# Optimization experiments

Measured on AMD Instinct MI355X. Metric: run time of the kernel, lower is better.

The kernel has to match this reference:

```python
import jax, jax.numpy as jnp
import numpy as np

N_NODES = 50000
N_EDGES = 400000
NUM_FEAT = 11
HID = 64
LAT = 64
HEADS = 3
MAX_NODES = 29
NUM_GRAPHS = 2048
NEG_SLOPE = 0.2


def _w(key, shape):
    return (jax.random.normal(key, shape) * 0.05).astype(jnp.float32)


def setup_inputs() -> dict:
    key = jax.random.key(0)
    ks = jax.random.split(key, 32)
    x = jax.random.normal(ks[0], (N_NODES, NUM_FEAT), dtype=jnp.float32)
    edge_index = jax.random.randint(ks[1], (2, N_EDGES), 0, N_NODES, dtype=jnp.int64)
    batch = jnp.sort(jax.random.randint(ks[2], (N_NODES,), 0, NUM_GRAPHS, dtype=jnp.int64))
    d = {"x": x, "edge_index": edge_index, "batch": batch}
    # GATv2 layer params: lin_l, lin_r ([in, heads*out]), att [heads,out], bias [out]
    dims = [(NUM_FEAT, HID), (HID, 2 * HID), (2 * HID, 4 * HID)]
    k = 3
    for i, (cin, cout) in enumerate(dims, start=1):
        d[f"Wl{i}"] = _w(ks[k], (cin, HEADS * cout)); k += 1
        d[f"bl{i}"] = jnp.zeros((HEADS * cout,), jnp.float32)
        d[f"Wr{i}"] = _w(ks[k], (cin, HEADS * cout)); k += 1
        d[f"br{i}"] = jnp.zeros((HEADS * cout,), jnp.float32)
        d[f"att{i}"] = _w(ks[k], (HEADS, cout)); k += 1
        d[f"b{i}"] = jnp.zeros((cout,), jnp.float32)
    d["Wmu"] = _w(ks[k], (4 * HID, LAT)); k += 1
    d["bmu"] = jnp.zeros((LAT,), jnp.float32)
    d["Wlv"] = _w(ks[k], (4 * HID, LAT)); k += 1
    d["blv"] = jnp.zeros((LAT,), jnp.float32)
    out_dim = MAX_NODES * NUM_FEAT + MAX_NODES * MAX_NODES
    d["Wd1"] = _w(ks[k], (LAT, 4 * HID)); k += 1
    d["bd1"] = jnp.zeros((4 * HID,), jnp.float32)
    d["Wd2"] = _w(ks[k], (4 * HID, 8 * HID)); k += 1
    d["bd2"] = jnp.zeros((8 * HID,), jnp.float32)
    d["Wd3"] = _w(ks[k], (8 * HID, out_dim)); k += 1
    d["bd3"] = jnp.zeros((out_dim,), jnp.float32)
    return d


def _gatv2(x, src, dst, Wl, bl, Wr, br, att, bias):
    # GATv2Conv, heads=HEADS, concat=False (mean over heads), self-loops already in src/dst
    N = x.shape[0]
    H, C = att.shape
    xl = (x @ Wl + bl).reshape(N, H, C)  # source transform
    xr = (x @ Wr + br).reshape(N, H, C)  # target transform
    e = jax.nn.leaky_relu(xl[src] + xr[dst], NEG_SLOPE)  # [E,H,C]
    logits = jnp.einsum('ehc,hc->eh', e, att)            # [E,H]
    mx = jax.ops.segment_max(logits, dst, num_segments=N)
    a = jnp.exp(logits - mx[dst])
    denom = jax.ops.segment_sum(a, dst, num_segments=N)
    alpha = a / (denom[dst] + 1e-16)
    out = jax.ops.segment_sum(alpha[:, :, None] * xl[src], dst, num_segments=N)  # [N,H,C]
    return out.mean(axis=1) + bias


def reference(x, edge_index, batch,
              Wl1, bl1, Wr1, br1, att1, b1,
              Wl2, bl2, Wr2, br2, att2, b2,
              Wl3, bl3, Wr3, br3, att3, b3,
              Wmu, bmu, Wlv, blv,
              Wd1, bd1, Wd2, bd2, Wd3, bd3):
    N = x.shape[0]
    loops = jnp.arange(N, dtype=edge_index.dtype)
    src = jnp.concatenate([edge_index[0], loops])
    dst = jnp.concatenate([edge_index[1], loops])
    h = jax.nn.relu(_gatv2(x, src, dst, Wl1, bl1, Wr1, br1, att1, b1))
    h = jax.nn.relu(_gatv2(h, src, dst, Wl2, bl2, Wr2, br2, att2, b2))
    h = jax.nn.relu(_gatv2(h, src, dst, Wl3, bl3, Wr3, br3, att3, b3))
    g = jax.ops.segment_sum(h, batch, num_segments=NUM_GRAPHS)  # global_add_pool
    mu = g @ Wmu + bmu
    logvar = g @ Wlv + blv
    z = mu  # deterministic decode of the posterior mean (no forward() given)
    o = jax.nn.relu(z @ Wd1 + bd1)
    o = jax.nn.relu(o @ Wd2 + bd2)
    o = o @ Wd3 + bd3
    nsplit = MAX_NODES * NUM_FEAT
    x_rec = o[:, :nsplit].reshape(-1, MAX_NODES, NUM_FEAT)
    adj = o[:, nsplit:].reshape(-1, MAX_NODES, MAX_NODES)
    adj_rec = (adj + jnp.swapaxes(adj, 1, 2)) / 2
    return (x_rec, adj_rec, mu, logvar)
```

## Files before the change

### kernel.cpp

```cpp
#include <hip/hip_runtime.h>
#include <hip/hip_bf16.h>

typedef __hip_bfloat16 bf16;
typedef unsigned short ushortT;
typedef ushortT u16x2 __attribute__((ext_vector_type(2)));
typedef ushortT u16x4 __attribute__((ext_vector_type(4)));
typedef ushortT u16x8 __attribute__((ext_vector_type(8)));
typedef __bf16   bf16x8 __attribute__((ext_vector_type(8)));
typedef float    f32x4  __attribute__((ext_vector_type(4)));

#define N_NODES    50000
#define E_EDGES    400000
#define E_TOT      450000
#define NUM_GRAPHS 2048
#define SCAN_CHUNK 1024
#define N_CHUNKS   ((N_NODES + SCAN_CHUNK - 1) / SCAN_CHUNK)

__device__ __forceinline__ float fromb(ushortT u) {
    unsigned int i = ((unsigned int)u) << 16;
    return __builtin_bit_cast(float, i);
}
__device__ __forceinline__ ushortT tob(float v) {
    bf16 h = __float2bfloat16(v);
    return __builtin_bit_cast(ushortT, h);
}

template <int VEC> struct RawV;
template <> struct RawV<1> { using T = ushortT; };
template <> struct RawV<2> { using T = u16x2; };
template <> struct RawV<4> { using T = u16x4; };

__device__ __forceinline__ void cvtv(ushortT r, float* f) { f[0] = fromb(r); }
__device__ __forceinline__ void cvtv(u16x2 r, float* f)   { f[0] = fromb(r.x); f[1] = fromb(r.y); }
__device__ __forceinline__ void cvtv(u16x4 r, float* f)   { f[0] = fromb(r.x); f[1] = fromb(r.y);
                                                            f[2] = fromb(r.z); f[3] = fromb(r.w); }

__global__ void diag_kernel(float* out, float v) { if (threadIdx.x == 0) out[0] = v; }

__global__ void hist_kernel(const int* __restrict__ ei, int* __restrict__ counts) {
    int e = blockIdx.x * 256 + threadIdx.x;
    if (e >= E_TOT) return;
    int d = (e < E_EDGES) ? ei[E_EDGES + e] : (e - E_EDGES);
    atomicAdd(&counts[d], 1);
}

__global__ __launch_bounds__(256) void scan_sums(const int* __restrict__ counts,
                                                 int* __restrict__ chunk_sums) {
    __shared__ int red[4];
    int base = blockIdx.x * SCAN_CHUNK;
    int t = threadIdx.x;
    int s = 0;
    #pragma unroll
    for (int i = 0; i < 4; i++) {
        int idx = base + t + i * 256;
        if (idx < N_NODES) s += counts[idx];
    }
    #pragma unroll
    for (int o = 32; o > 0; o >>= 1) s += __shfl_xor(s, o);
    if ((t & 63) == 0) red[t >> 6] = s;
    __syncthreads();
    if (t == 0) chunk_sums[blockIdx.x] = red[0] + red[1] + red[2] + red[3];
}

__global__ __launch_bounds__(64) void scan_chunks(const int* __restrict__ chunk_sums,
                                                  int* __restrict__ chunk_base) {
    int t = threadIdx.x;
    int v = (t < N_CHUNKS) ? chunk_sums[t] : 0;
    int orig = v;
    #pragma unroll
    for (int o = 1; o < 64; o <<= 1) {
        int u = __shfl_up(v, o);
        if (t >= o) v += u;
    }
    if (t < N_CHUNKS) chunk_base[t] = v - orig;
}

__global__ __launch_bounds__(256) void scan_write(const int* __restrict__ counts,
                                                  const int* __restrict__ chunk_base,
                                                  int* __restrict__ offsets) {
    __shared__ int wsum[4];
    int chunk = blockIdx.x;
    int base = chunk * SCAN_CHUNK;
    int t = threadIdx.x;
    int lane = t & 63, w = t >> 6;

    int c[4];
    int e0 = base + t * 4;
    #pragma unroll
    for (int k = 0; k < 4; k++) {
        int idx = e0 + k;
        c[k] = (idx < N_NODES) ? counts[idx] : 0;
    }
    int local = c[0] + c[1] + c[2] + c[3];

    int v = local;
    #pragma unroll
    for (int o = 1; o < 64; o <<= 1) {
        int u = __shfl_up(v, o);
        if (lane >= o) v += u;
    }
    if (lane == 63) wsum[w] = v;
    __syncthreads();
    int wbase = 0;
    for (int i = 0; i < w; i++) wbase += wsum[i];

    int run = chunk_base[chunk] + wbase + (v - local);
    #pragma unroll
    for (int k = 0; k < 4; k++) {
        int idx = e0 + k;
        if (idx < N_NODES) offsets[idx] = run;
        run += c[k];
    }
    if (chunk == 0 && t == 0) offsets[N_NODES] = E_TOT;
}

__global__ void copy_kernel(const int* __restrict__ src, int* __restrict__ dst, int n) {
    int i = blockIdx.x * 256 + threadIdx.x;
    if (i < n) dst[i] = src[i];
}

__global__ void scatter_kernel(const int* __restrict__ ei, int* __restrict__ cursor,
                               int* __restrict__ srcs) {
    int e = blockIdx.x * 256 + threadIdx.x;
    if (e >= E_TOT) return;
    int s, d;
    if (e < E_EDGES) { s = ei[e]; d = ei[E_EDGES + e]; }
    else             { s = d = e - E_EDGES; }
    int pos = atomicAdd(&cursor[d], 1);
    srcs[pos] = s;
}

__global__ void repack_kernel(const float* __restrict__ W, ushortT* __restrict__ Bp,
                              int K, int N) {
    int idx = blockIdx.x * 256 + threadIdx.x;
    if (idx >= K * N) return;
    int k = idx / N, n = idx % N;
    Bp[((size_t)(k >> 3) * N + n) * 8 + (k & 7)] = tob(W[idx]);
}

__global__ void repack_split(const float* __restrict__ W, ushortT* __restrict__ Bh,
                             ushortT* __restrict__ Bl, int K, int N, int Npad) {
    int idx = blockIdx.x * 256 + threadIdx.x;
    if (idx >= K * Npad) return;
    int k = idx / Npad, n = idx % Npad;
    float v = (n < N) ? W[(size_t)k * N + n] : 0.f;
    ushortT h = tob(v);
    float r = v - fromb(h);
    size_t o = ((size_t)(k >> 3) * Npad + n) * 8 + (k & 7);
    Bh[o] = h;
    Bl[o] = tob(r);
}

__global__ __launch_bounds__(192) void l1_transform(const float* __restrict__ x,
                                                    const float* __restrict__ Wl,
                                                    const float* __restrict__ bl,
                                                    const float* __restrict__ Wr,
                                                    const float* __restrict__ br,
                                                    ushortT* __restrict__ XL,
                                                    ushortT* __restrict__ XR, int M) {
    __shared__ float xs[64][11];
    const int tid = threadIdx.x;
    const int bm  = blockIdx.x * 64;
    const int rows = (M - bm < 64) ? (M - bm) : 64;

    float wl[11], wr[11];
    #pragma unroll
    for (int k = 0; k < 11; k++) {
        wl[k] = Wl[k * 192 + tid];
        wr[k] = Wr[k * 192 + tid];
    }
    float blc = bl[tid], brc = br[tid];

    for (int i = tid; i < rows * 11; i += 192)
        xs[i / 11][i % 11] = x[(size_t)bm * 11 + i];
    __syncthreads();

    for (int r = 0; r < rows; r++) {
        float al = blc, ar = brc;
        #pragma unroll
        for (int k = 0; k < 11; k++) {
            float xv = xs[r][k];
            al += xv * wl[k];
            ar += xv * wr[k];
        }
        size_t o = (size_t)(bm + r) * 192 + tid;
        XL[o] = tob(al);
        XR[o] = tob(ar);
    }
}

template <bool RELU>
__global__ __launch_bounds__(256) void gemm_dec(const float* __restrict__ A,
                                                const float* __restrict__ B,
                                                const float* __restrict__ bias,
                                                float* __restrict__ C,
                                                int M, int N, int K,
                                                int lda, int ldb, int ldc) {
    __shared__ float As[32][33];
    __shared__ float Bs[32][65];
    int tid = threadIdx.x;
    int tm = tid >> 4, tn = tid & 15;
    int bm = blockIdx.y * 32, bn = blockIdx.x * 64;
    float acc[2][4] = {};
    for (int k0 = 0; k0 < K; k0 += 32) {
        #pragma unroll
        for (int i = 0; i < 4; i++) {
            int e = tid + i * 256;
            int r = e >> 5, k = e & 31;
            int row = bm + r, kk = k0 + k;
            float v = 0.f;
            if (row < M && kk < K) v = A[(size_t)row * lda + kk];
            As[k][r] = v;
        }
        #pragma unroll
        for (int i = 0; i < 8; i++) {
            int e = tid + i * 256;
            int k = e >> 6, n = e & 63;
            int kk = k0 + k, col = bn + n;
            float v = 0.f;
            if (kk < K && col < N) v = B[(size_t)kk * ldb + col];
            Bs[k][n] = v;
        }
        __syncthreads();
        #pragma unroll
        for (int k = 0; k < 32; k++) {
            float a0 = As[k][tm * 2 + 0], a1 = As[k][tm * 2 + 1];
            float b0 = Bs[k][tn * 4 + 0], b1 = Bs[k][tn * 4 + 1];
            float b2 = Bs[k][tn * 4 + 2], b3 = Bs[k][tn * 4 + 3];
            acc[0][0] += a0 * b0; acc[0][1] += a0 * b1; acc[0][2] += a0 * b2; acc[0][3] += a0 * b3;
            acc[1][0] += a1 * b0; acc[1][1] += a1 * b1; acc[1][2] += a1 * b2; acc[1][3] += a1 * b3;
        }
        __syncthreads();
    }
    #pragma unroll
    for (int i = 0; i < 2; i++) {
        int row = bm + tm * 2 + i;
        if (row >= M) continue;
        #pragma unroll
        for (int j = 0; j < 4; j++) {
            int col = bn + tn * 4 + j;
            if (col >= N) continue;
            float v = acc[i][j] + bias[col];
            if (RELU) v = fmaxf(v, 0.f);
            C[(size_t)row * ldc + col] = v;
        }
    }
}

template <bool RELU>
__global__ __launch_bounds__(256) void mfma_dec(const float* __restrict__ A,
                                                const ushortT* __restrict__ Bh,
                                                const ushortT* __restrict__ Bl,
                                                const float* __restrict__ bias,
                                                float* __restrict__ C,
                                                int M, int N, int K, int Npad,
                                                int lda, int ldc) {
    __shared__ ushortT Ah[4 * 128 * 8];
    __shared__ ushortT Al[4 * 128 * 8];
    const int tid = threadIdx.x;
    const int bm = blockIdx.y * 128;
    const int bn = blockIdx.x * 128;
    const int lane = tid & 63;
    const int l15 = lane & 15, lg = lane >> 4;
    const int wid = tid >> 6;
    const int wm = wid >> 1, wn = wid & 1;

    f32x4 acc[4][4] = {};

    for (int k0 = 0; k0 < K; k0 += 32) {
        __syncthreads();
        #pragma unroll
        for (int it = 0; it < 2; it++) {
            int c = tid + it * 256;
            int row = c >> 2, kg = c & 3;
            const float* ap = A + (size_t)(bm + row) * lda + k0 + kg * 8;
            u16x8 hv, lv;
            #pragma unroll
            for (int i = 0; i < 8; i++) {
                float v = ap[i];
                ushortT h = tob(v);
                hv[i] = h;
                lv[i] = tob(v - fromb(h));
            }
            int unit = (kg * 128 + row) ^ kg;
            *reinterpret_cast<u16x8*>(&Ah[unit * 8]) = hv;
            *reinterpret_cast<u16x8*>(&Al[unit * 8]) = lv;
        }
        __syncthreads();

        bf16x8 ah[4], al[4], bhf[4], blf[4];
        #pragma unroll
        for (int mf = 0; mf < 4; mf++) {
            int row = wm * 64 + mf * 16 + l15;
            int unit = (lg * 128 + row) ^ lg;
            ah[mf] = __builtin_bit_cast(bf16x8, *reinterpret_cast<const u16x8*>(&Ah[unit * 8]));
            al[mf] = __builtin_bit_cast(bf16x8, *reinterpret_cast<const u16x8*>(&Al[unit * 8]));
        }
        int kgG = (k0 >> 3) + lg;
        #pragma unroll
        for (int nf = 0; nf < 4; nf++) {
            int n = bn + wn * 64 + nf * 16 + l15;
            size_t o = ((size_t)kgG * Npad + n) * 8;
            bhf[nf] = __builtin_bit_cast(bf16x8, *reinterpret_cast<const u16x8*>(Bh + o));
            blf[nf] = __builtin_bit_cast(bf16x8, *reinterpret_cast<const u16x8*>(Bl + o));
        }
        #pragma unroll
        for (int mf = 0; mf < 4; mf++) {
            #pragma unroll
            for (int nf = 0; nf < 4; nf++) {
                acc[mf][nf] = __builtin_amdgcn_mfma_f32_16x16x32_bf16(ah[mf], bhf[nf], acc[mf][nf], 0, 0, 0);
                acc[mf][nf] = __builtin_amdgcn_mfma_f32_16x16x32_bf16(ah[mf], blf[nf], acc[mf][nf], 0, 0, 0);
                acc[mf][nf] = __builtin_amdgcn_mfma_f32_16x16x32_bf16(al[mf], bhf[nf], acc[mf][nf], 0, 0, 0);
            }
        }
    }

    #pragma unroll
    for (int nf = 0; nf < 4; nf++) {
        int col = bn + wn * 64 + nf * 16 + l15;
        if (col >= N) continue;
        float bv = bias[col];
        #pragma unroll
        for (int mf = 0; mf < 4; mf++) {
            #pragma unroll
            for (int q = 0; q < 4; q++) {
                int row = bm + wm * 64 + mf * 16 + lg * 4 + q;
                if (row < M) {
                    float v = acc[mf][nf][q] + bv;
                    if (RELU) v = fmaxf(v, 0.f);
                    C[(size_t)row * ldc + col] = v;
                }
            }
        }
    }
}

template <int K, int CHH>
__global__ __launch_bounds__(256) void mfma_gemm(const ushortT* __restrict__ A,
                                                 const ushortT* __restrict__ BpL,
                                                 const ushortT* __restrict__ BpR,
                                                 const float* __restrict__ bl,
                                                 const float* __restrict__ br,
                                                 bf16* __restrict__ XL,
                                                 bf16* __restrict__ XR,
                                                 int M, int Nfull, int n0) {
    constexpr int KU = K / 8;
    __shared__ ushortT Alds[KU * 128 * 8];
    const int tid = threadIdx.x;
    const int bm  = blockIdx.y * 128;
    const int bnb = blockIdx.x * 128;

    for (int u = tid; u < 128 * KU; u += 256) {
        int row = u / KU, kg = u % KU;
        int rg = bm + row; if (rg > M - 1) rg = M - 1;
        u16x8 v = *reinterpret_cast<const u16x8*>(A + (size_t)rg * K + kg * 8);
        int unit = (kg * 128 + row) ^ (kg & 7);
        *reinterpret_cast<u16x8*>(&Alds[unit * 8]) = v;
    }
    __syncthreads();

    const int lane = tid & 63;
    const int l15 = lane & 15, lg = lane >> 4;
    const int wid = tid >> 6;
    const int wm = wid >> 1, wn = wid & 1;

    f32x4 acc[4][4] = {};
    #pragma unroll
    for (int s = 0; s < K / 32; s++) {
        int kg = s * 4 + lg;
        bf16x8 a[4], b[4];
        #pragma unroll
        for (int mf = 0; mf < 4; mf++) {
            int row = wm * 64 + mf * 16 + l15;
            int unit = (kg * 128 + row) ^ (kg & 7);
            a[mf] = __builtin_bit_cast(bf16x8,
                    *reinterpret_cast<const u16x8*>(&Alds[unit * 8]));
        }
        #pragma unroll
        for (int nf = 0; nf < 4; nf++) {
            int cb = bnb + wn * 64 + nf * 16;
            const ushortT* bp; int n;
            if (cb < CHH) { bp = BpL; n = n0 + cb + l15; }
            else          { bp = BpR; n = n0 + cb - CHH + l15; }
            b[nf] = __builtin_bit_cast(bf16x8,
                    *reinterpret_cast<const u16x8*>(bp + ((size_t)kg * Nfull + n) * 8));
        }
        #pragma unroll
        for (int mf = 0; mf < 4; mf++)
            #pragma unroll
            for (int nf = 0; nf < 4; nf++)
                acc[mf][nf] = __builtin_amdgcn_mfma_f32_16x16x32_bf16(
                    a[mf], b[nf], acc[mf][nf], 0, 0, 0);
    }

    #pragma unroll
    for (int nf = 0; nf < 4; nf++) {
        int cb = bnb + wn * 64 + nf * 16;
        bf16* Cp; const float* bs; int c;
        if (cb < CHH) { Cp = XL; bs = bl; c = cb + l15; }
        else          { Cp = XR; bs = br; c = cb - CHH + l15; }
        float bv = bs[c];
        #pragma unroll
        for (int mf = 0; mf < 4; mf++) {
            #pragma unroll
            for (int q = 0; q < 4; q++) {
                int r = bm + wm * 64 + mf * 16 + lg * 4 + q;
                if (r < M) Cp[(size_t)r * CHH + c] = __float2bfloat16(acc[mf][nf][q] + bv);
            }
        }
    }
}

template <int CHH, int MODE>
__global__ __launch_bounds__(256) void gat_head(const ushortT* __restrict__ XL,
                                                const ushortT* __restrict__ XR,
                                                int ldx, int offx,
                                                const float* __restrict__ att_h,
                                                const float* __restrict__ bias,
                                                const int* __restrict__ offsets,
                                                const int* __restrict__ srcs,
                                                ushortT* __restrict__ OUT, int N) {
    constexpr int VEC = CHH / 64;
    using RT = typename RawV<VEC>::T;
    int wid  = threadIdx.x >> 6;
    int lane = threadIdx.x & 63;
    int n = blockIdx.x * 4 + wid;
    if (n >= N) return;

    float xr_[VEC], a06[VEC], a04[VEC], acc[VEC];
    const ushortT* xrp = XR + (size_t)n * ldx + offx + VEC * lane;
    #pragma unroll
    for (int i = 0; i < VEC; i++) {
        xr_[i] = fromb(xrp[i]);
        float a = att_h[VEC * lane + i];
        a06[i] = 0.6f * a;
        a04[i] = 0.4f * a;
        acc[i] = 0.f;
    }
    float denom = 0.f;

    const int e0 = offsets[n], e1 = offsets[n + 1];
    const int deg = e1 - e0;
    const int loff = offx + VEC * lane;

    for (int base = 0; base < deg; base += 64) {
        int cnt = deg - base; if (cnt > 64) cnt = 64;
        int sl = srcs[e0 + base + ((lane < cnt) ? lane : (cnt - 1))];

        RT pf0, pf1, pf2, pf3;
        pf0 = *reinterpret_cast<const RT*>(XL + (size_t)__shfl(sl, 0) * ldx + loff);
        pf1 = (cnt > 1) ? *reinterpret_cast<const RT*>(XL + (size_t)__shfl(sl, 1) * ldx + loff) : pf0;
        pf2 = (cnt > 2) ? *reinterpret_cast<const RT*>(XL + (size_t)__shfl(sl, 2) * ldx + loff) : pf0;
        pf3 = (cnt > 3) ? *reinterpret_cast<const RT*>(XL + (size_t)__shfl(sl, 3) * ldx + loff) : pf0;

        for (int j = 0; j < cnt; ++j) {
            RT cur = pf0;
            pf0 = pf1; pf1 = pf2; pf2 = pf3;
            if (j + 4 < cnt)
                pf3 = *reinterpret_cast<const RT*>(XL + (size_t)__shfl(sl, j + 4) * ldx + loff);

            float xl[VEC];
            cvtv(cur, xl);
            float part = 0.f;
            #pragma unroll
            for (int i = 0; i < VEC; i++) {
                float v = xl[i] + xr_[i];
                float av = fabsf(v);
                part = fmaf(a06[i], v, part);
                part = fmaf(a04[i], av, part);
            }
            #pragma unroll
            for (int ofs = 32; ofs > 0; ofs >>= 1)
                part += __shfl_xor(part, ofs);

            float w = __expf(part);
            denom += w;
            #pragma unroll
            for (int i = 0; i < VEC; i++) acc[i] = fmaf(w, xl[i], acc[i]);
        }
    }

    float inv = 1.f / (denom + 1e-16f);
    #pragma unroll
    for (int i = 0; i < VEC; i++) {
        int c = VEC * lane + i;
        size_t idx = (size_t)n * CHH + c;
        float v = acc[i] * inv;
        if (MODE > 0) v += fromb(OUT[idx]);
        if (MODE == 2) { v = v * (1.f / 3.f) + bias[c]; v = fmaxf(v, 0.f); }
        OUT[idx] = tob(v);
    }
}

__global__ void pool_kernel(const ushortT* __restrict__ h3, const int* __restrict__ batch,
                            float* __restrict__ G) {
    int g = blockIdx.x;
    int c = threadIdx.x;
    int lo = 0, hi = N_NODES;
    while (lo < hi) { int mid = (lo + hi) >> 1; if (batch[mid] < g) lo = mid + 1; else hi = mid; }
    int s0 = lo;
    hi = N_NODES;
    while (lo < hi) { int mid = (lo + hi) >> 1; if (batch[mid] < g + 1) lo = mid + 1; else hi = mid; }
    int s1 = lo;
    float sum = 0.f;
    for (int n = s0; n < s1; n++) sum += fromb(h3[(size_t)n * 256 + c]);
    G[(size_t)g * 256 + c] = sum;
}

__global__ void assemble_kernel(const float* __restrict__ o3, float* __restrict__ out) {
    int g = blockIdx.x;
    const float* row = o3 + (size_t)g * 1160;
    float* xrec = out + (size_t)g * 319;
    for (int p = threadIdx.x; p < 319; p += 256) xrec[p] = row[p];
    float* adj = out + 653312 + (size_t)g * 841;
    for (int p = threadIdx.x; p < 841; p += 256) {
        int i = p / 29, j = p % 29;
        adj[p] = 0.5f * (row[319 + p] + row[319 + j * 29 + i]);
    }
}

extern "C" void kernel_launch(void* const* d_in, const int* in_sizes, int n_in,
                              void* d_out, int out_size, void* d_ws, size_t ws_size,
                              hipStream_t stream) {
    const float* x     = (const float*)d_in[0];
    const int*   ei    = (const int*)d_in[1];
    const int*   batch = (const int*)d_in[2];
    const float* Wl1 = (const float*)d_in[3];
    const float* bl1 = (const float*)d_in[4];
    const float* Wr1 = (const float*)d_in[5];
    const float* br1 = (const float*)d_in[6];
    const float* att1= (const float*)d_in[7];
    const float* b1  = (const float*)d_in[8];
    const float* Wl2 = (const float*)d_in[9];
    const float* bl2 = (const float*)d_in[10];
    const float* Wr2 = (const float*)d_in[11];
    const float* br2 = (const float*)d_in[12];
    const float* att2= (const float*)d_in[13];
    const float* b2  = (const float*)d_in[14];
    const float* Wl3 = (const float*)d_in[15];
    const float* bl3 = (const float*)d_in[16];
    const float* Wr3 = (const float*)d_in[17];
    const float* br3 = (const float*)d_in[18];
    const float* att3= (const float*)d_in[19];
    const float* b3  = (const float*)d_in[20];
    const float* Wmu = (const float*)d_in[21];
    const float* bmu = (const float*)d_in[22];
    const float* Wlv = (const float*)d_in[23];
    const float* blv = (const float*)d_in[24];
    const float* Wd1 = (const float*)d_in[25];
    const float* bd1 = (const float*)d_in[26];
    const float* Wd2 = (const float*)d_in[27];
    const float* bd2 = (const float*)d_in[28];
    const float* Wd3 = (const float*)d_in[29];
    const float* bd3 = (const float*)d_in[30];
    float* out = (float*)d_out;

    char* wsb = (char*)d_ws;
    ushortT* h3u = (ushortT*)(wsb + 0);
    ushortT* h1u = (ushortT*)(wsb + 0);
    ushortT* h2u = (ushortT*)(wsb + 25600000);
    bf16*    XLb = (bf16*)(wsb + 38400000);
    ushortT* XLu = (ushortT*)(wsb + 38400000);
    bf16*    XRb = (bf16*)(wsb + 64000000);
    ushortT* XRu = (ushortT*)(wsb + 64000000);
    float* G  = (float*)(wsb + 38400000);
    float* O1 = G  + 524288;
    float* O2 = O1 + 524288;
    float* O3 = O2 + 1048576;
    ushortT* BhD3 = (ushortT*)(wsb + 64000000);
    ushortT* BlD3 = (ushortT*)(wsb + 65400000);
    ushortT* BhD2 = (ushortT*)(wsb + 66800000);
    ushortT* BlD2 = (ushortT*)(wsb + 67100000);
    ushortT* BhD1 = (ushortT*)(wsb + 67400000);
    ushortT* BlD1 = (ushortT*)(wsb + 67500000);
    int* counts  = (int*)(wsb + 89600000);
    int* offsets = counts + (N_NODES + 1);
    int* cursor  = offsets + (N_NODES + 1);
    int* srcs    = cursor + (N_NODES + 1);
    int* chunk_sums = srcs + E_TOT;
    int* chunk_base = chunk_sums + 64;
    ushortT* BpL2 = (ushortT*)(wsb + 92000528);
    ushortT* BpR2 = (ushortT*)(wsb + 92049680);
    ushortT* BpL3 = (ushortT*)(wsb + 92098832);
    ushortT* BpR3 = (ushortT*)(wsb + 92295440);

    size_t needed = 92492048;
    if (ws_size < needed) {
        hipLaunchKernelGGL(diag_kernel, dim3(1), dim3(64), 0, stream, out, (float)(ws_size >> 20));
        return;
    }

    const int MU_OFF = 2375680;
    const int LV_OFF = 2506752;

    hipMemsetAsync(counts, 0, sizeof(int) * (N_NODES + 1), stream);
    hipLaunchKernelGGL(hist_kernel, dim3((E_TOT + 255) / 256), dim3(256), 0, stream, ei, counts);
    hipLaunchKernelGGL(scan_sums,   dim3(N_CHUNKS), dim3(256), 0, stream, counts, chunk_sums);
    hipLaunchKernelGGL(scan_chunks, dim3(1), dim3(64), 0, stream, chunk_sums, chunk_base);
    hipLaunchKernelGGL(scan_write,  dim3(N_CHUNKS), dim3(256), 0, stream,
                       counts, chunk_base, offsets);
    hipLaunchKernelGGL(copy_kernel, dim3((N_NODES + 255) / 256), dim3(256), 0, stream,
                       offsets, cursor, N_NODES);
    hipLaunchKernelGGL(scatter_kernel, dim3((E_TOT + 255) / 256), dim3(256), 0, stream,
                       ei, cursor, srcs);

    hipLaunchKernelGGL(repack_kernel, dim3((64 * 384 + 255) / 256), dim3(256), 0, stream,
                       Wl2, BpL2, 64, 384);
    hipLaunchKernelGGL(repack_kernel, dim3((64 * 384 + 255) / 256), dim3(256), 0, stream,
                       Wr2, BpR2, 64, 384);
    hipLaunchKernelGGL(repack_kernel, dim3((128 * 768 + 255) / 256), dim3(256), 0, stream,
                       Wl3, BpL3, 128, 768);
    hipLaunchKernelGGL(repack_kernel, dim3((128 * 768 + 255) / 256), dim3(256), 0, stream,
                       Wr3, BpR3, 128, 768);

    const dim3 AGG_GRID(N_NODES / 4);

    hipLaunchKernelGGL(l1_transform, dim3((N_NODES + 63) / 64), dim3(192), 0, stream,
                       x, Wl1, bl1, Wr1, br1, XLu, XRu, N_NODES);
    hipLaunchKernelGGL((gat_head<64, 0>), AGG_GRID, dim3(256), 0, stream,
                       XLu, XRu, 192, 0,   att1 + 0,   b1, offsets, srcs, h1u, N_NODES);
    hipLaunchKernelGGL((gat_head<64, 1>), AGG_GRID, dim3(256), 0, stream,
                       XLu, XRu, 192, 64,  att1 + 64,  b1, offsets, srcs, h1u, N_NODES);
    hipLaunchKernelGGL((gat_head<64, 2>), AGG_GRID, dim3(256), 0, stream,
                       XLu, XRu, 192, 128, att1 + 128, b1, offsets, srcs, h1u, N_NODES);

    for (int h = 0; h < 3; ++h) {
        hipLaunchKernelGGL((mfma_gemm<64, 128>), dim3(2, 391), dim3(256), 0, stream,
                           h1u, BpL2, BpR2, bl2 + h * 128, br2 + h * 128,
                           XLb, XRb, N_NODES, 384, h * 128);
        if (h == 0)      hipLaunchKernelGGL((gat_head<128, 0>), AGG_GRID, dim3(256), 0, stream,
                             XLu, XRu, 128, 0, att2 + h * 128, b2, offsets, srcs, h2u, N_NODES);
        else if (h == 1) hipLaunchKernelGGL((gat_head<128, 1>), AGG_GRID, dim3(256), 0, stream,
                             XLu, XRu, 128, 0, att2 + h * 128, b2, offsets, srcs, h2u, N_NODES);
        else             hipLaunchKernelGGL((gat_head<128, 2>), AGG_GRID, dim3(256), 0, stream,
                             XLu, XRu, 128, 0, att2 + h * 128, b2, offsets, srcs, h2u, N_NODES);
    }

    for (int h = 0; h < 3; ++h) {
        hipLaunchKernelGGL((mfma_gemm<128, 256>), dim3(4, 391), dim3(256), 0, stream,
                           h2u, BpL3, BpR3, bl3 + h * 256, br3 + h * 256,
                           XLb, XRb, N_NODES, 768, h * 256);
        if (h == 0)      hipLaunchKernelGGL((gat_head<256, 0>), AGG_GRID, dim3(256), 0, stream,
                             XLu, XRu, 256, 0, att3 + h * 256, b3, offsets, srcs, h3u, N_NODES);
        else if (h == 1) hipLaunchKernelGGL((gat_head<256, 1>), AGG_GRID, dim3(256), 0, stream,
                             XLu, XRu, 256, 0, att3 + h * 256, b3, offsets, srcs, h3u, N_NODES);
        else             hipLaunchKernelGGL((gat_head<256, 2>), AGG_GRID, dim3(256), 0, stream,
                             XLu, XRu, 256, 0, att3 + h * 256, b3, offsets, srcs, h3u, N_NODES);
    }

    hipLaunchKernelGGL(repack_split, dim3((64 * 256 + 255) / 256), dim3(256), 0, stream,
                       Wd1, BhD1, BlD1, 64, 256, 256);
    hipLaunchKernelGGL(repack_split, dim3((256 * 512 + 255) / 256), dim3(256), 0, stream,
                       Wd2, BhD2, BlD2, 256, 512, 512);
    hipLaunchKernelGGL(repack_split, dim3((512 * 1280 + 255) / 256), dim3(256), 0, stream,
                       Wd3, BhD3, BlD3, 512, 1160, 1280);

    hipLaunchKernelGGL(pool_kernel, dim3(NUM_GRAPHS), dim3(256), 0, stream, h3u, batch, G);

    hipLaunchKernelGGL((gemm_dec<false>), dim3(1, 64), dim3(256), 0, stream,
                       G, Wmu, bmu, out + MU_OFF, NUM_GRAPHS, 64, 256, 256, 64, 64);
    hipLaunchKernelGGL((gemm_dec<false>), dim3(1, 64), dim3(256), 0, stream,
                       G, Wlv, blv, out + LV_OFF, NUM_GRAPHS, 64, 256, 256, 64, 64);
    hipLaunchKernelGGL((mfma_dec<true>), dim3(2, 16), dim3(256), 0, stream,
                       out + MU_OFF, BhD1, BlD1, bd1, O1, NUM_GRAPHS, 256, 64, 256, 64, 256);
    hipLaunchKernelGGL((mfma_dec<true>), dim3(4, 16), dim3(256), 0, stream,
                       O1, BhD2, BlD2, bd2, O2, NUM_GRAPHS, 512, 256, 512, 256, 512);
    hipLaunchKernelGGL((mfma_dec<false>), dim3(10, 16), dim3(256), 0, stream,
                       O2, BhD3, BlD3, bd3, O3, NUM_GRAPHS, 1160, 512, 1280, 512, 1160);
    hipLaunchKernelGGL(assemble_kernel, dim3(NUM_GRAPHS), dim3(256), 0, stream, O3, out);
}
```

Measured before the change: 992.6 us.

## Fuse all three attention heads into one aggregation pass and one GEMM per layer

Replaces the per-head GEMM plus per-head aggregation launches with a single GEMM producing all heads' XL/XR and one aggregation kernel that processes all three heads per edge, reusing the gathered neighbour indices and writing the head-mean, bias and ReLU once. This removes repeated CSR traversal, repeated read-modify-write of the output, and many kernel launches. It also fuses the weight repack kernels and folds the cursor copy into the scan. In exchange it needs a larger workspace for full-width XL/XR buffers and holds more registers per thread, which may reduce occupancy.

```diff
diff --git a/kernel.cpp b/kernel.cpp
--- a/kernel.cpp
+++ b/kernel.cpp
@@ -3,6 +3,7 @@
 
 typedef __hip_bfloat16 bf16;
 typedef unsigned short ushortT;
+typedef ushortT u16x1 __attribute__((ext_vector_type(1)));
 typedef ushortT u16x2 __attribute__((ext_vector_type(2)));
 typedef ushortT u16x4 __attribute__((ext_vector_type(4)));
 typedef ushortT u16x8 __attribute__((ext_vector_type(8)));
@@ -26,14 +27,14 @@
 }
 
 template <int VEC> struct RawV;
-template <> struct RawV<1> { using T = ushortT; };
+template <> struct RawV<1> { using T = u16x1; };
 template <> struct RawV<2> { using T = u16x2; };
 template <> struct RawV<4> { using T = u16x4; };
 
-__device__ __forceinline__ void cvtv(ushortT r, float* f) { f[0] = fromb(r); }
-__device__ __forceinline__ void cvtv(u16x2 r, float* f)   { f[0] = fromb(r.x); f[1] = fromb(r.y); }
-__device__ __forceinline__ void cvtv(u16x4 r, float* f)   { f[0] = fromb(r.x); f[1] = fromb(r.y);
-                                                            f[2] = fromb(r.z); f[3] = fromb(r.w); }
+__device__ __forceinline__ void cvtv(u16x1 r, float* f) { f[0] = fromb(r[0]); }
+__device__ __forceinline__ void cvtv(u16x2 r, float* f) { f[0] = fromb(r.x); f[1] = fromb(r.y); }
+__device__ __forceinline__ void cvtv(u16x4 r, float* f) { f[0] = fromb(r.x); f[1] = fromb(r.y);
+                                                          f[2] = fromb(r.z); f[3] = fromb(r.w); }
 
 __global__ void diag_kernel(float* out, float v) { if (threadIdx.x == 0) out[0] = v; }
 
@@ -77,7 +78,8 @@
 
 __global__ __launch_bounds__(256) void scan_write(const int* __restrict__ counts,
                                                   const int* __restrict__ chunk_base,
-                                                  int* __restrict__ offsets) {
+                                                  int* __restrict__ offsets,
+                                                  int* __restrict__ cursor) {
     __shared__ int wsum[4];
     int chunk = blockIdx.x;
     int base = chunk * SCAN_CHUNK;
@@ -108,15 +110,10 @@
     #pragma unroll
     for (int k = 0; k < 4; k++) {
         int idx = e0 + k;
-        if (idx < N_NODES) offsets[idx] = run;
+        if (idx < N_NODES) { offsets[idx] = run; cursor[idx] = run; }
         run += c[k];
     }
     if (chunk == 0 && t == 0) offsets[N_NODES] = E_TOT;
-}
-
-__global__ void copy_kernel(const int* __restrict__ src, int* __restrict__ dst, int n) {
-    int i = blockIdx.x * 256 + threadIdx.x;
-    if (i < n) dst[i] = src[i];
 }
 
 __global__ void scatter_kernel(const int* __restrict__ ei, int* __restrict__ cursor,
@@ -130,25 +127,40 @@
     srcs[pos] = s;
 }
 
-__global__ void repack_kernel(const float* __restrict__ W, ushortT* __restrict__ Bp,
-                              int K, int N) {
+__global__ void repack_gat_kernel(const float* __restrict__ Wl2, const float* __restrict__ Wr2,
+                                  const float* __restrict__ Wl3, const float* __restrict__ Wr3,
+                                  ushortT* __restrict__ BpL2, ushortT* __restrict__ BpR2,
+                                  ushortT* __restrict__ BpL3, ushortT* __restrict__ BpR3) {
+    const int S2 = 64 * 384, S3 = 128 * 768;
     int idx = blockIdx.x * 256 + threadIdx.x;
-    if (idx >= K * N) return;
-    int k = idx / N, n = idx % N;
-    Bp[((size_t)(k >> 3) * N + n) * 8 + (k & 7)] = tob(W[idx]);
-}
-
-__global__ void repack_split(const float* __restrict__ W, ushortT* __restrict__ Bh,
-                             ushortT* __restrict__ Bl, int K, int N, int Npad) {
+    const float* W; ushortT* Bp; int N, local;
+    if (idx < S2)                { W = Wl2; Bp = BpL2; N = 384; local = idx; }
+    else if (idx < 2 * S2)       { W = Wr2; Bp = BpR2; N = 384; local = idx - S2; }
+    else if (idx < 2 * S2 + S3)  { W = Wl3; Bp = BpL3; N = 768; local = idx - 2 * S2; }
+    else if (idx < 2 * (S2 + S3)){ W = Wr3; Bp = BpR3; N = 768; local = idx - 2 * S2 - S3; }
+    else return;
+    int k = local / N, n = local % N;
+    Bp[((size_t)(k >> 3) * N + n) * 8 + (k & 7)] = tob(W[(size_t)k * N + n]);
+}
+
+__global__ void repack_split3(const float* __restrict__ Wd1, const float* __restrict__ Wd2,
+                              const float* __restrict__ Wd3,
+                              ushortT* __restrict__ BhD1, ushortT* __restrict__ BlD1,
+                              ushortT* __restrict__ BhD2, ushortT* __restrict__ BlD2,
+                              ushortT* __restrict__ BhD3, ushortT* __restrict__ BlD3) {
+    const int T1 = 64 * 256, T2 = 256 * 512, T3 = 512 * 1280;
     int idx = blockIdx.x * 256 + threadIdx.x;
-    if (idx >= K * Npad) return;
-    int k = idx / Npad, n = idx % Npad;
+    const float* W; ushortT *Bh, *Bl; int Npad, N, local;
+    if (idx < T1)                { W = Wd1; Bh = BhD1; Bl = BlD1; Npad = 256;  N = 256;  local = idx; }
+    else if (idx < T1 + T2)      { W = Wd2; Bh = BhD2; Bl = BlD2; Npad = 512;  N = 512;  local = idx - T1; }
+    else if (idx < T1 + T2 + T3) { W = Wd3; Bh = BhD3; Bl = BlD3; Npad = 1280; N = 1160; local = idx - T1 - T2; }
+    else return;
+    int k = local / Npad, n = local % Npad;
     float v = (n < N) ? W[(size_t)k * N + n] : 0.f;
     ushortT h = tob(v);
-    float r = v - fromb(h);
     size_t o = ((size_t)(k >> 3) * Npad + n) * 8 + (k & 7);
     Bh[o] = h;
-    Bl[o] = tob(r);
+    Bl[o] = tob(v - fromb(h));
 }
 
 __global__ __launch_bounds__(192) void l1_transform(const float* __restrict__ x,
@@ -335,15 +347,15 @@
     }
 }
 
-template <int K, int CHH>
-__global__ __launch_bounds__(256) void mfma_gemm(const ushortT* __restrict__ A,
-                                                 const ushortT* __restrict__ BpL,
-                                                 const ushortT* __restrict__ BpR,
-                                                 const float* __restrict__ bl,
-                                                 const float* __restrict__ br,
-                                                 bf16* __restrict__ XL,
-                                                 bf16* __restrict__ XR,
-                                                 int M, int Nfull, int n0) {
+template <int K, int NW>
+__global__ __launch_bounds__(256) void mfma_gemmF(const ushortT* __restrict__ A,
+                                                  const ushortT* __restrict__ BpL,
+                                                  const ushortT* __restrict__ BpR,
+                                                  const float* __restrict__ bl,
+                                                  const float* __restrict__ br,
+                                                  bf16* __restrict__ XL,
+                                                  bf16* __restrict__ XR,
+                                                  int M) {
     constexpr int KU = K / 8;
     __shared__ ushortT Alds[KU * 128 * 8];
     const int tid = threadIdx.x;
@@ -380,10 +392,10 @@
         for (int nf = 0; nf < 4; nf++) {
             int cb = bnb + wn * 64 + nf * 16;
             const ushortT* bp; int n;
-            if (cb < CHH) { bp = BpL; n = n0 + cb + l15; }
-            else          { bp = BpR; n = n0 + cb - CHH + l15; }
+            if (cb < NW) { bp = BpL; n = cb + l15; }
+            else         { bp = BpR; n = cb - NW + l15; }
             b[nf] = __builtin_bit_cast(bf16x8,
-                    *reinterpret_cast<const u16x8*>(bp + ((size_t)kg * Nfull + n) * 8));
+                    *reinterpret_cast<const u16x8*>(bp + ((size_t)kg * NW + n) * 8));
         }
         #pragma unroll
         for (int mf = 0; mf < 4; mf++)
@@ -397,99 +409,132 @@
     for (int nf = 0; nf < 4; nf++) {
         int cb = bnb + wn * 64 + nf * 16;
         bf16* Cp; const float* bs; int c;
-        if (cb < CHH) { Cp = XL; bs = bl; c = cb + l15; }
-        else          { Cp = XR; bs = br; c = cb - CHH + l15; }
+        if (cb < NW) { Cp = XL; bs = bl; c = cb + l15; }
+        else         { Cp = XR; bs = br; c = cb - NW + l15; }
         float bv = bs[c];
         #pragma unroll
         for (int mf = 0; mf < 4; mf++) {
             #pragma unroll
             for (int q = 0; q < 4; q++) {
                 int r = bm + wm * 64 + mf * 16 + lg * 4 + q;
-                if (r < M) Cp[(size_t)r * CHH + c] = __float2bfloat16(acc[mf][nf][q] + bv);
-            }
-        }
-    }
-}
-
-template <int CHH, int MODE>
-__global__ __launch_bounds__(256) void gat_head(const ushortT* __restrict__ XL,
-                                                const ushortT* __restrict__ XR,
-                                                int ldx, int offx,
-                                                const float* __restrict__ att_h,
-                                                const float* __restrict__ bias,
-                                                const int* __restrict__ offsets,
-                                                const int* __restrict__ srcs,
-                                                ushortT* __restrict__ OUT, int N) {
+                if (r < M) Cp[(size_t)r * NW + c] = __float2bfloat16(acc[mf][nf][q] + bv);
+            }
+        }
+    }
+}
+
+template <int CHH>
+__global__ __launch_bounds__(256) void gat_fused(const ushortT* __restrict__ XL,
+                                                 const ushortT* __restrict__ XR,
+                                                 const float* __restrict__ att,
+                                                 const float* __restrict__ bias,
+                                                 const int* __restrict__ offsets,
+                                                 const int* __restrict__ srcs,
+                                                 ushortT* __restrict__ OUT, int N) {
     constexpr int VEC = CHH / 64;
+    constexpr int LDX = 3 * CHH;
     using RT = typename RawV<VEC>::T;
     int wid  = threadIdx.x >> 6;
     int lane = threadIdx.x & 63;
     int n = blockIdx.x * 4 + wid;
     if (n >= N) return;
 
-    float xr_[VEC], a06[VEC], a04[VEC], acc[VEC];
-    const ushortT* xrp = XR + (size_t)n * ldx + offx + VEC * lane;
-    #pragma unroll
-    for (int i = 0; i < VEC; i++) {
-        xr_[i] = fromb(xrp[i]);
-        float a = att_h[VEC * lane + i];
-        a06[i] = 0.6f * a;
-        a04[i] = 0.4f * a;
-        acc[i] = 0.f;
-    }
-    float denom = 0.f;
-
-    const int e0 = offsets[n], e1 = offsets[n + 1];
-    const int deg = e1 - e0;
-    const int loff = offx + VEC * lane;
+    const int loff = VEC * lane;
+    float xr_[3][VEC], a06[3][VEC], a04[3][VEC], acc[3][VEC];
+    const ushortT* xrp = XR + (size_t)n * LDX + loff;
+    #pragma unroll
+    for (int h = 0; h < 3; h++) {
+        RT xrv = *reinterpret_cast<const RT*>(xrp + h * CHH);
+        #pragma unroll
+        for (int i = 0; i < VEC; i++) {
+            xr_[h][i] = fromb(xrv[i]);
+            float a = att[h * CHH + loff + i];
+            a06[h][i] = 0.6f * a;
+            a04[h][i] = 0.4f * a;
+            acc[h][i] = 0.f;
+        }
+    }
+    float d0 = 0.f, d1 = 0.f, d2 = 0.f;
+
+    const int e0 = offsets[n];
+    const int deg = offsets[n + 1] - e0;
 
     for (int base = 0; base < deg; base += 64) {
         int cnt = deg - base; if (cnt > 64) cnt = 64;
         int sl = srcs[e0 + base + ((lane < cnt) ? lane : (cnt - 1))];
 
-        RT pf0, pf1, pf2, pf3;
-        pf0 = *reinterpret_cast<const RT*>(XL + (size_t)__shfl(sl, 0) * ldx + loff);
-        pf1 = (cnt > 1) ? *reinterpret_cast<const RT*>(XL + (size_t)__shfl(sl, 1) * ldx + loff) : pf0;
-        pf2 = (cnt > 2) ? *reinterpret_cast<const RT*>(XL + (size_t)__shfl(sl, 2) * ldx + loff) : pf0;
-        pf3 = (cnt > 3) ? *reinterpret_cast<const RT*>(XL + (size_t)__shfl(sl, 3) * ldx + loff) : pf0;
+        RT A0, A1, A2, B0, B1, B2, C0, C1, C2;
+        {
+            const ushortT* r = XL + (size_t)__shfl(sl, 0) * LDX + loff;
+            A0 = *reinterpret_cast<const RT*>(r);
+            A1 = *reinterpret_cast<const RT*>(r + CHH);
+            A2 = *reinterpret_cast<const RT*>(r + 2 * CHH);
+        }
+        if (cnt > 1) {
+            const ushortT* r = XL + (size_t)__shfl(sl, 1) * LDX + loff;
+            B0 = *reinterpret_cast<const RT*>(r);
+            B1 = *reinterpret_cast<const RT*>(r + CHH);
+            B2 = *reinterpret_cast<const RT*>(r + 2 * CHH);
+        } else { B0 = A0; B1 = A1; B2 = A2; }
+        if (cnt > 2) {
+            const ushortT* r = XL + (size_t)__shfl(sl, 2) * LDX + loff;
+            C0 = *reinterpret_cast<const RT*>(r);
+            C1 = *reinterpret_cast<const RT*>(r + CHH);
+            C2 = *reinterpret_cast<const RT*>(r + 2 * CHH);
+        } else { C0 = A0; C1 = A1; C2 = A2; }
 
         for (int j = 0; j < cnt; ++j) {
-            RT cur = pf0;
-            pf0 = pf1; pf1 = pf2; pf2 = pf3;
-            if (j + 4 < cnt)
-                pf3 = *reinterpret_cast<const RT*>(XL + (size_t)__shfl(sl, j + 4) * ldx + loff);
-
-            float xl[VEC];
-            cvtv(cur, xl);
-            float part = 0.f;
+            RT c0 = A0, c1 = A1, c2 = A2;
+            A0 = B0; A1 = B1; A2 = B2;
+            B0 = C0; B1 = C1; B2 = C2;
+            if (j + 3 < cnt) {
+                const ushortT* r = XL + (size_t)__shfl(sl, j + 3) * LDX + loff;
+                C0 = *reinterpret_cast<const RT*>(r);
+                C1 = *reinterpret_cast<const RT*>(r + CHH);
+                C2 = *reinterpret_cast<const RT*>(r + 2 * CHH);
+            }
+
+            float xl0[VEC], xl1[VEC], xl2[VEC];
+            cvtv(c0, xl0); cvtv(c1, xl1); cvtv(c2, xl2);
+            float p0 = 0.f, p1 = 0.f, p2 = 0.f;
             #pragma unroll
             for (int i = 0; i < VEC; i++) {
-                float v = xl[i] + xr_[i];
-                float av = fabsf(v);
-                part = fmaf(a06[i], v, part);
-                part = fmaf(a04[i], av, part);
-            }
-            #pragma unroll
-            for (int ofs = 32; ofs > 0; ofs >>= 1)
-                part += __shfl_xor(part, ofs);
-
-            float w = __expf(part);
-            denom += w;
-            #pragma unroll
-            for (int i = 0; i < VEC; i++) acc[i] = fmaf(w, xl[i], acc[i]);
-        }
-    }
-
-    float inv = 1.f / (denom + 1e-16f);
+                float v0 = xl0[i] + xr_[0][i];
+                float v1 = xl1[i] + xr_[1][i];
+                float v2 = xl2[i] + xr_[2][i];
+                p0 = fmaf(a06[0][i], v0, p0); p0 = fmaf(a04[0][i], fabsf(v0), p0);
+                p1 = fmaf(a06[1][i], v1, p1); p1 = fmaf(a04[1][i], fabsf(v1), p1);
+                p2 = fmaf(a06[2][i], v2, p2); p2 = fmaf(a04[2][i], fabsf(v2), p2);
+            }
+            #pragma unroll
+            for (int ofs = 32; ofs > 0; ofs >>= 1) {
+                p0 += __shfl_xor(p0, ofs);
+                p1 += __shfl_xor(p1, ofs);
+                p2 += __shfl_xor(p2, ofs);
+            }
+
+            float w0 = __expf(p0), w1 = __expf(p1), w2 = __expf(p2);
+            d0 += w0; d1 += w1; d2 += w2;
+            #pragma unroll
+            for (int i = 0; i < VEC; i++) {
+                acc[0][i] = fmaf(w0, xl0[i], acc[0][i]);
+                acc[1][i] = fmaf(w1, xl1[i], acc[1][i]);
+                acc[2][i] = fmaf(w2, xl2[i], acc[2][i]);
+            }
+        }
+    }
+
+    float i0 = 1.f / (d0 + 1e-16f);
+    float i1 = 1.f / (d1 + 1e-16f);
+    float i2 = 1.f / (d2 + 1e-16f);
+    RT ov;
     #pragma unroll
     for (int i = 0; i < VEC; i++) {
-        int c = VEC * lane + i;
-        size_t idx = (size_t)n * CHH + c;
-        float v = acc[i] * inv;
-        if (MODE > 0) v += fromb(OUT[idx]);
-        if (MODE == 2) { v = v * (1.f / 3.f) + bias[c]; v = fmaxf(v, 0.f); }
-        OUT[idx] = tob(v);
-    }
+        int c = loff + i;
+        float v = (acc[0][i] * i0 + acc[1][i] * i1 + acc[2][i] * i2) * (1.f / 3.f) + bias[c];
+        ov[i] = tob(fmaxf(v, 0.f));
+    }
+    *reinterpret_cast<RT*>(&OUT[(size_t)n * CHH + loff]) = ov;
 }
 
 __global__ void pool_kernel(const ushortT* __restrict__ h3, const int* __restrict__ batch,
@@ -555,105 +600,73 @@
     const float* bd3 = (const float*)d_in[30];
     float* out = (float*)d_out;
 
+    const int MU_OFF = 2375680;
+    const int LV_OFF = 2506752;
     char* wsb = (char*)d_ws;
+
+    const size_t NEED_FULL = 194892064;
+    const dim3 AGG_GRID(N_NODES / 4);
+
+    if (ws_size < NEED_FULL) {
+        hipLaunchKernelGGL(diag_kernel, dim3(1), dim3(64), 0, stream, out, (float)(ws_size >> 20));
+        return;
+    }
+
     ushortT* h3u = (ushortT*)(wsb + 0);
     ushortT* h1u = (ushortT*)(wsb + 0);
     ushortT* h2u = (ushortT*)(wsb + 25600000);
     bf16*    XLb = (bf16*)(wsb + 38400000);
     ushortT* XLu = (ushortT*)(wsb + 38400000);
-    bf16*    XRb = (bf16*)(wsb + 64000000);
-    ushortT* XRu = (ushortT*)(wsb + 64000000);
+    bf16*    XRb = (bf16*)(wsb + 115200000);
+    ushortT* XRu = (ushortT*)(wsb + 115200000);
     float* G  = (float*)(wsb + 38400000);
     float* O1 = G  + 524288;
     float* O2 = O1 + 524288;
     float* O3 = O2 + 1048576;
-    ushortT* BhD3 = (ushortT*)(wsb + 64000000);
-    ushortT* BlD3 = (ushortT*)(wsb + 65400000);
-    ushortT* BhD2 = (ushortT*)(wsb + 66800000);
-    ushortT* BlD2 = (ushortT*)(wsb + 67100000);
-    ushortT* BhD1 = (ushortT*)(wsb + 67400000);
-    ushortT* BlD1 = (ushortT*)(wsb + 67500000);
-    int* counts  = (int*)(wsb + 89600000);
+    ushortT* BhD3 = (ushortT*)(wsb + 115200000);
+    ushortT* BlD3 = (ushortT*)(wsb + 116600000);
+    ushortT* BhD2 = (ushortT*)(wsb + 118000000);
+    ushortT* BlD2 = (ushortT*)(wsb + 118300000);
+    ushortT* BhD1 = (ushortT*)(wsb + 118600000);
+    ushortT* BlD1 = (ushortT*)(wsb + 118700000);
+    int* counts  = (int*)(wsb + 192000000);
     int* offsets = counts + (N_NODES + 1);
     int* cursor  = offsets + (N_NODES + 1);
     int* srcs    = cursor + (N_NODES + 1);
     int* chunk_sums = srcs + E_TOT;
     int* chunk_base = chunk_sums + 64;
-    ushortT* BpL2 = (ushortT*)(wsb + 92000528);
-    ushortT* BpR2 = (ushortT*)(wsb + 92049680);
-    ushortT* BpL3 = (ushortT*)(wsb + 92098832);
-    ushortT* BpR3 = (ushortT*)(wsb + 92295440);
-
-    size_t needed = 92492048;
-    if (ws_size < needed) {
-        hipLaunchKernelGGL(diag_kernel, dim3(1), dim3(64), 0, stream, out, (float)(ws_size >> 20));
-        return;
-    }
-
-    const int MU_OFF = 2375680;
-    const int LV_OFF = 2506752;
+    ushortT* BpL2 = (ushortT*)(wsb + 194400544);
+    ushortT* BpR2 = (ushortT*)(wsb + 194449696);
+    ushortT* BpL3 = (ushortT*)(wsb + 194498848);
+    ushortT* BpR3 = (ushortT*)(wsb + 194695456);
 
     hipMemsetAsync(counts, 0, sizeof(int) * (N_NODES + 1), stream);
     hipLaunchKernelGGL(hist_kernel, dim3((E_TOT + 255) / 256), dim3(256), 0, stream, ei, counts);
     hipLaunchKernelGGL(scan_sums,   dim3(N_CHUNKS), dim3(256), 0, stream, counts, chunk_sums);
     hipLaunchKernelGGL(scan_chunks, dim3(1), dim3(64), 0, stream, chunk_sums, chunk_base);
     hipLaunchKernelGGL(scan_write,  dim3(N_CHUNKS), dim3(256), 0, stream,
-                       counts, chunk_base, offsets);
-    hipLaunchKernelGGL(copy_kernel, dim3((N_NODES + 255) / 256), dim3(256), 0, stream,
-                       offsets, cursor, N_NODES);
+                       counts, chunk_base, offsets, cursor);
     hipLaunchKernelGGL(scatter_kernel, dim3((E_TOT + 255) / 256), dim3(256), 0, stream,
                        ei, cursor, srcs);
 
-    hipLaunchKernelGGL(repack_kernel, dim3((64 * 384 + 255) / 256), dim3(256), 0, stream,
-                       Wl2, BpL2, 64, 384);
-    hipLaunchKernelGGL(repack_kernel, dim3((64 * 384 + 255) / 256), dim3(256), 0, stream,
-                       Wr2, BpR2, 64, 384);
-    hipLaunchKernelGGL(repack_kernel, dim3((128 * 768 + 255) / 256), dim3(256), 0, stream,
-                       Wl3, BpL3, 128, 768);
-    hipLaunchKernelGGL(repack_kernel, dim3((128 * 768 + 255) / 256), dim3(256), 0, stream,
-                       Wr3, BpR3, 128, 768);
-
-    const dim3 AGG_GRID(N_NODES / 4);
+    hipLaunchKernelGGL(repack_gat_kernel, dim3(960), dim3(256), 0, stream,
+                       Wl2, Wr2, Wl3, Wr3, BpL2, BpR2, BpL3, BpR3);
 
     hipLaunchKernelGGL(l1_transform, dim3((N_NODES + 63) / 64), dim3(192), 0, stream,
                        x, Wl1, bl1, Wr1, br1, XLu, XRu, N_NODES);
-    hipLaunchKernelGGL((gat_head<64, 0>), AGG_GRID, dim3(256), 0, stream,
-                       XLu, XRu, 192, 0,   att1 + 0,   b1, offsets, srcs, h1u, N_NODES);
-    hipLaunchKernelGGL((gat_head<64, 1>), AGG_GRID, dim3(256), 0, stream,
-                       XLu, XRu, 192, 64,  att1 + 64,  b1, offsets, srcs, h1u, N_NODES);
-    hipLaunchKernelGGL((gat_head<64, 2>), AGG_GRID, dim3(256), 0, stream,
-                       XLu, XRu, 192, 128, att1 + 128, b1, offsets, srcs, h1u, N_NODES);
-
-    for (int h = 0; h < 3; ++h) {
-        hipLaunchKernelGGL((mfma_gemm<64, 128>), dim3(2, 391), dim3(256), 0, stream,
-                           h1u, BpL2, BpR2, bl2 + h * 128, br2 + h * 128,
-                           XLb, XRb, N_NODES, 384, h * 128);
-        if (h == 0)      hipLaunchKernelGGL((gat_head<128, 0>), AGG_GRID, dim3(256), 0, stream,
-                             XLu, XRu, 128, 0, att2 + h * 128, b2, offsets, srcs, h2u, N_NODES);
-        else if (h == 1) hipLaunchKernelGGL((gat_head<128, 1>), AGG_GRID, dim3(256), 0, stream,
-                             XLu, XRu, 128, 0, att2 + h * 128, b2, offsets, srcs, h2u, N_NODES);
-        else             hipLaunchKernelGGL((gat_head<128, 2>), AGG_GRID, dim3(256), 0, stream,
-                             XLu, XRu, 128, 0, att2 + h * 128, b2, offsets, srcs, h2u, N_NODES);
-    }
-
-    for (int h = 0; h < 3; ++h) {
-        hipLaunchKernelGGL((mfma_gemm<128, 256>), dim3(4, 391), dim3(256), 0, stream,
-                           h2u, BpL3, BpR3, bl3 + h * 256, br3 + h * 256,
-                           XLb, XRb, N_NODES, 768, h * 256);
-        if (h == 0)      hipLaunchKernelGGL((gat_head<256, 0>), AGG_GRID, dim3(256), 0, stream,
-                             XLu, XRu, 256, 0, att3 + h * 256, b3, offsets, srcs, h3u, N_NODES);
-        else if (h == 1) hipLaunchKernelGGL((gat_head<256, 1>), AGG_GRID, dim3(256), 0, stream,
-                             XLu, XRu, 256, 0, att3 + h * 256, b3, offsets, srcs, h3u, N_NODES);
-        else             hipLaunchKernelGGL((gat_head<256, 2>), AGG_GRID, dim3(256), 0, stream,
-                             XLu, XRu, 256, 0, att3 + h * 256, b3, offsets, srcs, h3u, N_NODES);
-    }
-
-    hipLaunchKernelGGL(repack_split, dim3((64 * 256 + 255) / 256), dim3(256), 0, stream,
-                       Wd1, BhD1, BlD1, 64, 256, 256);
-    hipLaunchKernelGGL(repack_split, dim3((256 * 512 + 255) / 256), dim3(256), 0, stream,
-                       Wd2, BhD2, BlD2, 256, 512, 512);
-    hipLaunchKernelGGL(repack_split, dim3((512 * 1280 + 255) / 256), dim3(256), 0, stream,
-                       Wd3, BhD3, BlD3, 512, 1160, 1280);
+    hipLaunchKernelGGL((gat_fused<64>), AGG_GRID, dim3(256), 0, stream,
+                       XLu, XRu, att1, b1, offsets, srcs, h1u, N_NODES);
+    hipLaunchKernelGGL((mfma_gemmF<64, 384>), dim3(6, 391), dim3(256), 0, stream,
+                       h1u, BpL2, BpR2, bl2, br2, XLb, XRb, N_NODES);
+    hipLaunchKernelGGL((gat_fused<128>), AGG_GRID, dim3(256), 0, stream,
+                       XLu, XRu, att2, b2, offsets, srcs, h2u, N_NODES);
+    hipLaunchKernelGGL((mfma_gemmF<128, 768>), dim3(12, 391), dim3(256), 0, stream,
+                       h2u, BpL3, BpR3, bl3, br3, XLb, XRb, N_NODES);
+    hipLaunchKernelGGL((gat_fused<256>), AGG_GRID, dim3(256), 0, stream,
+                       XLu, XRu, att3, b3, offsets, srcs, h3u, N_NODES);
+
+    hipLaunchKernelGGL(repack_split3, dim3(3136), dim3(256), 0, stream,
+                       Wd1, Wd2, Wd3, BhD1, BlD1, BhD2, BlD2, BhD3, BlD3);
 
     hipLaunchKernelGGL(pool_kernel, dim3(NUM_GRAPHS), dim3(256), 0, stream, h3u, batch, G);
 
```

New measurement: 833.5 us. -16.0%, faster.
